# Performance work log

Measured on AMD Instinct MI355X. Metric: run time of the kernel, lower is better.

Reference implementation:

```python
import jax, jax.numpy as jnp
import numpy as np

B, L, H, C, A = 8, 4096, 512, 64, 512
NEG = -1000000000.0

def setup_inputs() -> dict:
    key = jax.random.key(0)
    ks = jax.random.split(key, 6)
    hidden_states = jax.random.normal(ks[0], (B, L, H), dtype=jnp.float32)
    critical_mask = jax.random.randint(ks[1], (B, L, 1), 0, 2).astype(bool)
    count_active_channels = jax.random.randint(ks[2], (B, L, 1), 0, 64).astype(jnp.int32)
    channel_activity = jax.random.normal(ks[3], (B, L, C), dtype=jnp.float32)
    proj_w = jax.random.normal(ks[4], (H, A), dtype=jnp.float32) * 0.02
    proj_b = jnp.zeros((A,), dtype=jnp.float32)
    score_w = jax.random.normal(ks[5], (A, 1), dtype=jnp.float32) * 0.02
    score_b = jnp.zeros((1,), dtype=jnp.float32)
    return {"hidden_states": hidden_states, "critical_mask": critical_mask,
            "count_active_channels": count_active_channels,
            "channel_activity": channel_activity,
            "proj_w": proj_w, "proj_b": proj_b,
            "score_w": score_w, "score_b": score_b}

def reference(hidden_states, critical_mask, count_active_channels, channel_activity,
              proj_w, proj_b, score_w, score_b):
    mask = critical_mask[..., 0].astype(bool)                       # (B,L)
    count_signal = count_active_channels[..., 0].astype(hidden_states.dtype)  # (B,L)
    activity = jnp.maximum(channel_activity.astype(hidden_states.dtype), 0.0)  # (B,L,C)
    # score(tanh(proj(h)))  -> (B,L)
    logits = (jnp.tanh(hidden_states @ proj_w + proj_b) @ score_w + score_b)[..., 0]
    logits = logits + jnp.log1p(jnp.maximum(count_signal, 0.0))
    channel_mask = activity > 0                                      # (B,L,C)
    # (B,C,L) masked logits with log1p activity bias
    channel_logits = logits[:, None, :] + jnp.log1p(jnp.swapaxes(activity, 1, 2))
    channel_logits = jnp.where(jnp.swapaxes(channel_mask, 1, 2), channel_logits, NEG)
    has_channel_any = channel_mask.any(axis=1)                       # (B,C)
    weights = jax.nn.softmax(channel_logits, axis=-1)                # (B,C,L)
    weights = jnp.where(has_channel_any[..., None], weights, 0.0)
    channel_contexts = jnp.einsum('bcl,blh->bch', weights, hidden_states)  # (B,C,H)
    fallback = jnp.broadcast_to(hidden_states[:, -1:, :], channel_contexts.shape)
    channel_contexts = jnp.where(has_channel_any[..., None], channel_contexts, fallback)
    mix = activity / jnp.maximum(activity.sum(axis=2, keepdims=True), 1.0)  # (B,L,C)
    expanded_context = jnp.einsum('blc,bch->blh', mix, channel_contexts)    # (B,L,H)
    max_count = jnp.maximum(count_signal.max(axis=1, keepdims=True), 1.0)
    density_gate = 1.0 + count_signal / max_count                    # (B,L)
    attended = jnp.where(mask[..., None], expanded_context * density_gate[..., None], hidden_states)
    return attended, weights
```

## Files before the change

kernel.cpp:

```cpp
#include <hip/hip_runtime.h>
#include <hip/hip_bf16.h>
#include <math.h>

#define NEGV (-1000000000.0f)
constexpr int Bb = 8, Ll = 4096, Hh = 512, Cc = 64, Aa = 512;

typedef float f32x4 __attribute__((ext_vector_type(4)));
typedef short s16x8 __attribute__((ext_vector_type(8)));

__device__ inline ushort f2bf(float f) {
  union { float f; uint u; } v; v.f = f;
  uint u = v.u;
  return (ushort)((u + 0x7FFFu + ((u >> 16) & 1u)) >> 16);
}

__device__ inline uint bfpack2(float x, float y) {
  __hip_bfloat162 h = __float22bfloat162_rn(make_float2(x, y));
  union { __hip_bfloat162 h; uint u; } v; v.h = h;
  return v.u;
}

__global__ void k_init(const int* __restrict__ cnt, const float* __restrict__ sb,
                       float* __restrict__ logits, int* __restrict__ cmax) {
  int i = blockIdx.x * 256 + threadIdx.x;
  int c = cnt[i];
  logits[i] = sb[0] + log1pf(fmaxf((float)c, 0.f));
  int m = c;
#pragma unroll
  for (int s = 32; s; s >>= 1) m = max(m, __shfl_xor(m, s));
  if ((threadIdx.x & 63) == 0) atomicMax(&cmax[i >> 12], m);
}

__global__ void kT_pw(const float* __restrict__ pw, ushort* __restrict__ pwT) {
  __shared__ ushort s[64][65];
  const int k0 = (blockIdx.x >> 3) * 64, a0 = (blockIdx.x & 7) * 64;
  const int t = threadIdx.x;
#pragma unroll
  for (int i = 0; i < 16; ++i) {
    int e = t + i * 256;
    int kk = e >> 6, aa = e & 63;
    s[aa][kk] = f2bf(pw[(size_t)(k0 + kk) * Aa + a0 + aa]);
  }
  __syncthreads();
#pragma unroll
  for (int i = 0; i < 16; ++i) {
    int e = t + i * 256;
    int aa = e >> 6, kk = e & 63;
    pwT[(size_t)(a0 + aa) * Hh + k0 + kk] = s[aa][kk];
  }
}

__global__ __launch_bounds__(256) void k0_gemm(
    const float* __restrict__ hid, const ushort* __restrict__ pwT,
    const float* __restrict__ pb, const float* __restrict__ sw,
    float* __restrict__ logits) {
  __shared__ ushort At[128 * 40];
  __shared__ ushort Bt[128 * 40];
  const int bm = blockIdx.x, bn = blockIdx.y;
  const int tid = threadIdx.x;
  const int lane = tid & 63;
  const int w = tid >> 6;
  const int wm = w >> 1, wn = w & 1;
  const int lc = lane & 15, lq = lane >> 4;

  const int sr = tid >> 1;
  const int sk = (tid & 1) * 16;

  const float* Ag = hid + ((size_t)(bm * 128 + sr)) * Hh + sk;
  const ushort* Bg = pwT + ((size_t)(bn * 128 + sr)) * Hh + sk;

  f32x4 acc[4][4];
#pragma unroll
  for (int mi = 0; mi < 4; ++mi)
#pragma unroll
    for (int ni = 0; ni < 4; ++ni) acc[mi][ni] = (f32x4){0.f, 0.f, 0.f, 0.f};

  int aoff[4], boff[4];
#pragma unroll
  for (int i = 0; i < 4; ++i) {
    aoff[i] = (wm * 64 + i * 16 + lc) * 40 + lq * 8;
    boff[i] = (wn * 64 + i * 16 + lc) * 40 + lq * 8;
  }

  float4 a0 = *(const float4*)(Ag + 0), a1 = *(const float4*)(Ag + 4),
         a2 = *(const float4*)(Ag + 8), a3 = *(const float4*)(Ag + 12);
  uint4 b0 = *(const uint4*)(Bg + 0), b1 = *(const uint4*)(Bg + 8);

  for (int kb = 0; kb < 16; ++kb) {
    __syncthreads();
    uint4 p0 = {bfpack2(a0.x, a0.y), bfpack2(a0.z, a0.w),
                bfpack2(a1.x, a1.y), bfpack2(a1.z, a1.w)};
    uint4 p1 = {bfpack2(a2.x, a2.y), bfpack2(a2.z, a2.w),
                bfpack2(a3.x, a3.y), bfpack2(a3.z, a3.w)};
    *(uint4*)(At + sr * 40 + sk) = p0;
    *(uint4*)(At + sr * 40 + sk + 8) = p1;
    *(uint4*)(Bt + sr * 40 + sk) = b0;
    *(uint4*)(Bt + sr * 40 + sk + 8) = b1;
    __syncthreads();
    if (kb < 15) {
      const float* ag = Ag + (kb + 1) * 32;
      const ushort* bg = Bg + (kb + 1) * 32;
      a0 = *(const float4*)(ag + 0); a1 = *(const float4*)(ag + 4);
      a2 = *(const float4*)(ag + 8); a3 = *(const float4*)(ag + 12);
      b0 = *(const uint4*)(bg + 0); b1 = *(const uint4*)(bg + 8);
    }
    s16x8 af[4], bf[4];
#pragma unroll
    for (int mi = 0; mi < 4; ++mi) af[mi] = *(const s16x8*)(At + aoff[mi]);
#pragma unroll
    for (int ni = 0; ni < 4; ++ni) bf[ni] = *(const s16x8*)(Bt + boff[ni]);
#pragma unroll
    for (int mi = 0; mi < 4; ++mi)
#pragma unroll
      for (int ni = 0; ni < 4; ++ni)
        acc[mi][ni] = __builtin_amdgcn_mfma_f32_16x16x32_bf16(
            af[mi], bf[ni], acc[mi][ni], 0, 0, 0);
  }

  float pbv[4], swv[4];
#pragma unroll
  for (int ni = 0; ni < 4; ++ni) {
    int n = bn * 128 + wn * 64 + ni * 16 + lc;
    pbv[ni] = pb[n];
    swv[ni] = sw[n];
  }
#pragma unroll
  for (int mi = 0; mi < 4; ++mi) {
#pragma unroll
    for (int r = 0; r < 4; ++r) {
      float s = 0.f;
#pragma unroll
      for (int ni = 0; ni < 4; ++ni) {
        float x = acc[mi][ni][r] + pbv[ni];
        float e = __expf(2.f * x);
        float th = 1.f - 2.f / (e + 1.f);
        s = fmaf(th, swv[ni], s);
      }
      s += __shfl_xor(s, 1);
      s += __shfl_xor(s, 2);
      s += __shfl_xor(s, 4);
      s += __shfl_xor(s, 8);
      if (lc == 0) {
        int m = bm * 128 + wm * 64 + mi * 16 + lq * 4 + r;
        atomicAdd(&logits[m], s);
      }
    }
  }
}

__global__ void k2_transpose(const float* __restrict__ act,
                             float* __restrict__ actT,
                             float* __restrict__ dinv) {
  __shared__ float t64[64][65];
  const int b = blockIdx.x >> 6;
  const int l0 = (blockIdx.x & 63) * 64;
  const int tid = threadIdx.x;
#pragma unroll
  for (int i = 0; i < 16; ++i) {
    int e = tid + i * 256;
    int l = e >> 6, c = e & 63;
    float v = act[((size_t)(b * Ll + l0 + l)) * Cc + c];
    t64[l][c] = fmaxf(v, 0.f);
  }
  __syncthreads();
  if (tid < 64) {
    float s = 0.f;
#pragma unroll 8
    for (int c = 0; c < 64; ++c) s += t64[tid][c];
    dinv[b * Ll + l0 + tid] = 1.0f / fmaxf(s, 1.0f);
  }
#pragma unroll
  for (int i = 0; i < 16; ++i) {
    int e = tid + i * 256;
    int c = e >> 6, lq = e & 63;
    actT[((size_t)(b * Cc + c)) * Ll + l0 + lq] = t64[lq][c];
  }
}

__global__ void k3_softmax(const float* __restrict__ actT,
                           const float* __restrict__ logits,
                           float* __restrict__ wout,
                           ushort* __restrict__ wb16,
                           int* __restrict__ hasany) {
  __shared__ float rmax[4], rcnt[4], rsum[4];
  const int bid = blockIdx.x;
  const int b = bid >> 6;
  const int tid = threadIdx.x;
  const float* arow = actT + (size_t)bid * Ll;

  float xs[16];
  float lmax = NEGV, fcnt = 0.f;
#pragma unroll
  for (int i = 0; i < 16; ++i) {
    int l = tid + i * 256;
    float a = arow[l];
    float x;
    if (a > 0.f) {
      x = logits[b * Ll + l] + log1pf(a);
      fcnt += 1.f;
    } else {
      x = NEGV;
    }
    xs[i] = x;
    lmax = fmaxf(lmax, x);
  }
#pragma unroll
  for (int m = 32; m >= 1; m >>= 1) {
    lmax = fmaxf(lmax, __shfl_xor(lmax, m));
    fcnt += __shfl_xor(fcnt, m);
  }
  if ((tid & 63) == 0) { rmax[tid >> 6] = lmax; rcnt[tid >> 6] = fcnt; }
  __syncthreads();
  float m4 = fmaxf(fmaxf(rmax[0], rmax[1]), fmaxf(rmax[2], rmax[3]));
  float call = rcnt[0] + rcnt[1] + rcnt[2] + rcnt[3];

  float lsum = 0.f;
#pragma unroll
  for (int i = 0; i < 16; ++i) {
    float e = expf(xs[i] - m4);
    xs[i] = e;
    lsum += e;
  }
#pragma unroll
  for (int m = 32; m >= 1; m >>= 1) lsum += __shfl_xor(lsum, m);
  if ((tid & 63) == 0) rsum[tid >> 6] = lsum;
  __syncthreads();
  float s = rsum[0] + rsum[1] + rsum[2] + rsum[3];
  int any = call > 0.5f;
  float inv = any ? 1.0f / s : 0.f;
#pragma unroll
  for (int i = 0; i < 16; ++i) {
    float wv = xs[i] * inv;
    wout[(size_t)bid * Ll + tid + i * 256] = wv;
    wb16[(size_t)bid * Ll + tid + i * 256] = f2bf(wv);
  }
  if (tid == 0) hasany[bid] = any;
}

__global__ __launch_bounds__(256) void k5_mfma(
    const ushort* __restrict__ wb16, const float* __restrict__ hid,
    float* __restrict__ pbuf) {
  const int b = blockIdx.x, nt = blockIdx.y, kz = blockIdx.z;
  const int tid = threadIdx.x;
  const int w = tid >> 6, lane = tid & 63;
  const int lc = lane & 15, lq = lane >> 4;
  const int h0 = nt * 128 + w * 32;

  f32x4 acc[4][2];
#pragma unroll
  for (int mi = 0; mi < 4; ++mi)
#pragma unroll
    for (int ni = 0; ni < 2; ++ni) acc[mi][ni] = (f32x4){0.f, 0.f, 0.f, 0.f};

  const ushort* Abase =
      wb16 + (size_t)b * Cc * Ll + (size_t)lc * Ll + kz * 256 + lq * 8;
  const float* Bbase =
      hid + ((size_t)(b * Ll + kz * 256 + lq * 8)) * Hh + h0 + lc;

  for (int kb = 0; kb < 8; ++kb) {
    s16x8 af[4];
#pragma unroll
    for (int mi = 0; mi < 4; ++mi)
      af[mi] = *(const s16x8*)(Abase + (size_t)mi * 16 * Ll + kb * 32);
    s16x8 bf[2];
#pragma unroll
    for (int ni = 0; ni < 2; ++ni) {
      const float* bp = Bbase + (size_t)kb * 32 * Hh + ni * 16;
      uint u0 = bfpack2(bp[0 * Hh], bp[1 * Hh]);
      uint u1 = bfpack2(bp[2 * Hh], bp[3 * Hh]);
      uint u2 = bfpack2(bp[4 * Hh], bp[5 * Hh]);
      uint u3 = bfpack2(bp[6 * Hh], bp[7 * Hh]);
      union { uint4 u4; s16x8 s; } cv;
      cv.u4 = (uint4){u0, u1, u2, u3};
      bf[ni] = cv.s;
    }
#pragma unroll
    for (int mi = 0; mi < 4; ++mi)
#pragma unroll
      for (int ni = 0; ni < 2; ++ni)
        acc[mi][ni] = __builtin_amdgcn_mfma_f32_16x16x32_bf16(
            af[mi], bf[ni], acc[mi][ni], 0, 0, 0);
  }

  const size_t obase = ((size_t)(kz * Bb + b)) * Cc * Hh;
#pragma unroll
  for (int mi = 0; mi < 4; ++mi)
#pragma unroll
    for (int ni = 0; ni < 2; ++ni)
#pragma unroll
      for (int r = 0; r < 4; ++r)
        pbuf[obase + (size_t)(mi * 16 + lq * 4 + r) * Hh + h0 + ni * 16 + lc] =
            acc[mi][ni][r];
}

__global__ void k6_reduce(const float* __restrict__ pbuf,
                          const int* __restrict__ hasany,
                          const float* __restrict__ hid,
                          float* __restrict__ cctx) {
  int idx = blockIdx.x * 256 + threadIdx.x;
  float s = 0.f;
#pragma unroll
  for (int z = 0; z < 16; ++z) s += pbuf[(size_t)z * 262144 + idx];
  int bc = idx >> 9, b = idx >> 15, h = idx & 511;
  cctx[idx] = hasany[bc] ? s : hid[((size_t)(b * Ll + Ll - 1)) * Hh + h];
}

__global__ __launch_bounds__(256, 2) void k7_out(
    const float* __restrict__ hid, const float* __restrict__ act,
    const float* __restrict__ dinv, const float* __restrict__ cctx,
    const int* __restrict__ mask, const int* __restrict__ cnt,
    const int* __restrict__ cmax, float* __restrict__ out) {
  __shared__ float mix[32 * 68];
  __shared__ float gateb[32];
  __shared__ int maskb[32];
  const int b = blockIdx.x;
  const int l0 = blockIdx.y * 32;
  const int tid = threadIdx.x;
  const float maxcf = fmaxf((float)cmax[b], 1.0f);

#pragma unroll
  for (int i = 0; i < 2; ++i) {
    int q = tid + i * 256;
    int t = q >> 4, cq = q & 15;
    float4 a4 = *(const float4*)(act + ((size_t)(b * Ll + l0 + t)) * Cc + cq * 4);
    float dv = dinv[b * Ll + l0 + t];
    a4.x = fmaxf(a4.x, 0.f) * dv;
    a4.y = fmaxf(a4.y, 0.f) * dv;
    a4.z = fmaxf(a4.z, 0.f) * dv;
    a4.w = fmaxf(a4.w, 0.f) * dv;
    *(float4*)(mix + t * 68 + cq * 4) = a4;
  }
  if (tid < 32) {
    int l = l0 + tid;
    maskb[tid] = mask[b * Ll + l];
    gateb[tid] = 1.0f + (float)cnt[b * Ll + l] / maxcf;
  }
  __syncthreads();

  const int tt = tid >> 6;
  const int h = (tid & 63) * 8;
  float acc[8][8];
#pragma unroll
  for (int t = 0; t < 8; ++t)
#pragma unroll
    for (int u = 0; u < 8; ++u) acc[t][u] = 0.f;

#pragma unroll 4
  for (int c = 0; c < 64; ++c) {
    float4 cA = *(const float4*)(cctx + ((size_t)(b * Cc + c)) * Hh + h);
    float4 cB = *(const float4*)(cctx + ((size_t)(b * Cc + c)) * Hh + h + 4);
    float cv[8] = {cA.x, cA.y, cA.z, cA.w, cB.x, cB.y, cB.z, cB.w};
#pragma unroll
    for (int t = 0; t < 8; ++t) {
      float mv = mix[(tt * 8 + t) * 68 + c];
#pragma unroll
      for (int u = 0; u < 8; ++u) acc[t][u] = fmaf(mv, cv[u], acc[t][u]);
    }
  }
#pragma unroll
  for (int t = 0; t < 8; ++t) {
    int tok = tt * 8 + t;
    size_t off = ((size_t)(b * Ll + l0 + tok)) * Hh + h;
    float4 o1, o2;
    if (maskb[tok]) {
      float g = gateb[tok];
      o1 = make_float4(acc[t][0] * g, acc[t][1] * g, acc[t][2] * g, acc[t][3] * g);
      o2 = make_float4(acc[t][4] * g, acc[t][5] * g, acc[t][6] * g, acc[t][7] * g);
    } else {
      o1 = *(const float4*)(hid + off);
      o2 = *(const float4*)(hid + off + 4);
    }
    *(float4*)(out + off) = o1;
    *(float4*)(out + off + 4) = o2;
  }
}

extern "C" void kernel_launch(void* const* d_in, const int* in_sizes, int n_in,
                              void* d_out, int out_size, void* d_ws,
                              size_t ws_size, hipStream_t stream) {
  const float* hid = (const float*)d_in[0];
  const int* mask = (const int*)d_in[1];
  const int* cnt = (const int*)d_in[2];
  const float* act = (const float*)d_in[3];
  const float* pw = (const float*)d_in[4];
  const float* pb = (const float*)d_in[5];
  const float* sw = (const float*)d_in[6];
  const float* sb = (const float*)d_in[7];

  float* out_att = (float*)d_out;
  float* out_w = out_att + (size_t)Bb * Ll * Hh;

  float* ws = (float*)d_ws;
  float* cctx = ws;
  int* cmaxi = (int*)(ws + 262144);
  float* logits = ws + 262152;
  float* actT = ws + 294920;
  float* dinv = ws + 2392072;
  int* hasany = (int*)(ws + 2424840);
  ushort* pwT = (ushort*)(ws + 2425352);
  ushort* wb16 = (ushort*)(ws + 2556424);
  float* pbuf = ws + 3605000;

  hipMemsetAsync(cmaxi, 0, 8 * sizeof(int), stream);

  k_init<<<128, 256, 0, stream>>>(cnt, sb, logits, cmaxi);
  kT_pw<<<64, 256, 0, stream>>>(pw, pwT);
  k0_gemm<<<dim3(256, 4), 256, 0, stream>>>(hid, pwT, pb, sw, logits);
  k2_transpose<<<512, 256, 0, stream>>>(act, actT, dinv);
  k3_softmax<<<512, 256, 0, stream>>>(actT, logits, out_w, wb16, hasany);
  k5_mfma<<<dim3(8, 4, 16), 256, 0, stream>>>(wb16, hid, pbuf);
  k6_reduce<<<1024, 256, 0, stream>>>(pbuf, hasany, hid, cctx);
  k7_out<<<dim3(8, 128), 256, 0, stream>>>(hid, act, dinv, cctx, mask, cnt,
                                           cmaxi, out_att);
}
```

Baseline: 271.2 us.

## Pre-convert hidden states to bf16 and stream GEMM tiles via global_load_lds double buffering

Adds a separate kernel that converts hidden_states to bf16 once, using the attended output buffer as scratch. The projection GEMM then loads bf16 tiles straight into LDS with global_load_lds into a double-buffered, unpadded layout, instead of converting fp32 in registers inside every n-block. This cuts the fp32 hidden reads repeated across the four column blocks and overlaps loads with MFMA. In exchange it adds an extra pass over hidden_states plus a write, and the unpadded LDS layout may cause bank conflicts.

```diff
diff --git a/kernel.cpp b/kernel.cpp
--- a/kernel.cpp
+++ b/kernel.cpp
@@ -18,6 +18,27 @@
   __hip_bfloat162 h = __float22bfloat162_rn(make_float2(x, y));
   union { __hip_bfloat162 h; uint u; } v; v.h = h;
   return v.u;
+}
+
+__device__ __forceinline__ void gl16(const void* g, void* l) {
+  __builtin_amdgcn_global_load_lds(
+      reinterpret_cast<const __attribute__((address_space(1))) unsigned int*>(
+          reinterpret_cast<uintptr_t>(g)),
+      reinterpret_cast<__attribute__((address_space(3))) unsigned int*>(
+          reinterpret_cast<uintptr_t>(l)),
+      16, 0, 0);
+}
+
+__global__ void k_cvt(const float* __restrict__ hid, ushort* __restrict__ hidb) {
+  size_t i = (size_t)blockIdx.x * 256 + threadIdx.x;
+#pragma unroll
+  for (int r = 0; r < 4; ++r, i += 524288) {
+    const float4* p = (const float4*)(hid + i * 8);
+    float4 x = p[0], y = p[1];
+    uint4 u = {bfpack2(x.x, x.y), bfpack2(x.z, x.w),
+               bfpack2(y.x, y.y), bfpack2(y.z, y.w)};
+    *(uint4*)(hidb + i * 8) = u;
+  }
 }
 
 __global__ void k_init(const int* __restrict__ cnt, const float* __restrict__ sb,
@@ -51,11 +72,10 @@
 }
 
 __global__ __launch_bounds__(256) void k0_gemm(
-    const float* __restrict__ hid, const ushort* __restrict__ pwT,
+    const ushort* __restrict__ hidb, const ushort* __restrict__ pwT,
     const float* __restrict__ pb, const float* __restrict__ sw,
     float* __restrict__ logits) {
-  __shared__ ushort At[128 * 40];
-  __shared__ ushort Bt[128 * 40];
+  __shared__ ushort smem[16384];
   const int bm = blockIdx.x, bn = blockIdx.y;
   const int tid = threadIdx.x;
   const int lane = tid & 63;
@@ -63,11 +83,11 @@
   const int wm = w >> 1, wn = w & 1;
   const int lc = lane & 15, lq = lane >> 4;
 
-  const int sr = tid >> 1;
-  const int sk = (tid & 1) * 16;
-
-  const float* Ag = hid + ((size_t)(bm * 128 + sr)) * Hh + sk;
-  const ushort* Bg = pwT + ((size_t)(bn * 128 + sr)) * Hh + sk;
+  const int srow = tid >> 2;
+  const int schunk = (tid & 3) * 8;
+  const ushort* Ag = hidb + ((size_t)(bm * 128 + srow)) * Hh + schunk;
+  const ushort* Bg = pwT + ((size_t)(bn * 128 + srow)) * Hh + schunk;
+  const int wrow = 16 * w;
 
   f32x4 acc[4][4];
 #pragma unroll
@@ -75,47 +95,46 @@
 #pragma unroll
     for (int ni = 0; ni < 4; ++ni) acc[mi][ni] = (f32x4){0.f, 0.f, 0.f, 0.f};
 
-  int aoff[4], boff[4];
-#pragma unroll
-  for (int i = 0; i < 4; ++i) {
-    aoff[i] = (wm * 64 + i * 16 + lc) * 40 + lq * 8;
-    boff[i] = (wn * 64 + i * 16 + lc) * 40 + lq * 8;
-  }
-
-  float4 a0 = *(const float4*)(Ag + 0), a1 = *(const float4*)(Ag + 4),
-         a2 = *(const float4*)(Ag + 8), a3 = *(const float4*)(Ag + 12);
-  uint4 b0 = *(const uint4*)(Bg + 0), b1 = *(const uint4*)(Bg + 8);
-
+  const int aoffc = (wm * 64 + lc) * 32 + lq * 8;
+  const int boffc = (wn * 64 + lc) * 32 + lq * 8;
+
+#define K0_STAGE(buf, kb)                                   \
+  do {                                                      \
+    const ushort* ag = Ag + (kb) * 32;                      \
+    const ushort* bg = Bg + (kb) * 32;                      \
+    ushort* la = smem + (buf) * 4096 + wrow * 32;           \
+    ushort* lb = smem + 8192 + (buf) * 4096 + wrow * 32;    \
+    gl16(ag, la);                                           \
+    gl16(ag + 64 * Hh, la + 64 * 32);                       \
+    gl16(bg, lb);                                           \
+    gl16(bg + 64 * Hh, lb + 64 * 32);                       \
+  } while (0)
+
+  K0_STAGE(0, 0);
+  __syncthreads();
+
+  int buf = 0;
   for (int kb = 0; kb < 16; ++kb) {
-    __syncthreads();
-    uint4 p0 = {bfpack2(a0.x, a0.y), bfpack2(a0.z, a0.w),
-                bfpack2(a1.x, a1.y), bfpack2(a1.z, a1.w)};
-    uint4 p1 = {bfpack2(a2.x, a2.y), bfpack2(a2.z, a2.w),
-                bfpack2(a3.x, a3.y), bfpack2(a3.z, a3.w)};
-    *(uint4*)(At + sr * 40 + sk) = p0;
-    *(uint4*)(At + sr * 40 + sk + 8) = p1;
-    *(uint4*)(Bt + sr * 40 + sk) = b0;
-    *(uint4*)(Bt + sr * 40 + sk + 8) = b1;
-    __syncthreads();
-    if (kb < 15) {
-      const float* ag = Ag + (kb + 1) * 32;
-      const ushort* bg = Bg + (kb + 1) * 32;
-      a0 = *(const float4*)(ag + 0); a1 = *(const float4*)(ag + 4);
-      a2 = *(const float4*)(ag + 8); a3 = *(const float4*)(ag + 12);
-      b0 = *(const uint4*)(bg + 0); b1 = *(const uint4*)(bg + 8);
-    }
-    s16x8 af[4], bf[4];
-#pragma unroll
-    for (int mi = 0; mi < 4; ++mi) af[mi] = *(const s16x8*)(At + aoff[mi]);
-#pragma unroll
-    for (int ni = 0; ni < 4; ++ni) bf[ni] = *(const s16x8*)(Bt + boff[ni]);
+    if (kb < 15) K0_STAGE(buf ^ 1, kb + 1);
+    const ushort* Ab = smem + buf * 4096;
+    const ushort* Bt = smem + 8192 + buf * 4096;
+    s16x8 af[4], bfr[4];
+#pragma unroll
+    for (int mi = 0; mi < 4; ++mi)
+      af[mi] = *(const s16x8*)(Ab + aoffc + mi * 512);
+#pragma unroll
+    for (int ni = 0; ni < 4; ++ni)
+      bfr[ni] = *(const s16x8*)(Bt + boffc + ni * 512);
 #pragma unroll
     for (int mi = 0; mi < 4; ++mi)
 #pragma unroll
       for (int ni = 0; ni < 4; ++ni)
         acc[mi][ni] = __builtin_amdgcn_mfma_f32_16x16x32_bf16(
-            af[mi], bf[ni], acc[mi][ni], 0, 0, 0);
-  }
+            af[mi], bfr[ni], acc[mi][ni], 0, 0, 0);
+    __syncthreads();
+    buf ^= 1;
+  }
+#undef K0_STAGE
 
   float pbv[4], swv[4];
 #pragma unroll
@@ -401,11 +420,14 @@
   ushort* wb16 = (ushort*)(ws + 2556424);
   float* pbuf = ws + 3605000;
 
+  ushort* hidb = (ushort*)out_att;
+
   hipMemsetAsync(cmaxi, 0, 8 * sizeof(int), stream);
 
+  k_cvt<<<2048, 256, 0, stream>>>(hid, hidb);
   k_init<<<128, 256, 0, stream>>>(cnt, sb, logits, cmaxi);
   kT_pw<<<64, 256, 0, stream>>>(pw, pwT);
-  k0_gemm<<<dim3(256, 4), 256, 0, stream>>>(hid, pwT, pb, sw, logits);
+  k0_gemm<<<dim3(256, 4), 256, 0, stream>>>(hidb, pwT, pb, sw, logits);
   k2_transpose<<<512, 256, 0, stream>>>(act, actT, dinv);
   k3_softmax<<<512, 256, 0, stream>>>(actT, logits, out_w, wb16, hasany);
   k5_mfma<<<dim3(8, 4, 16), 256, 0, stream>>>(wb16, hid, pbuf);
```

New measurement: 276.7 us. +2.0%, slower.
